# Kernel optimization log

Hardware: AMD Instinct MI355X
Metric: run time of the kernel (lower is better)

The kernel has to match this reference:

```python
import jax, jax.numpy as jnp
import numpy as np

TOP_K = 8


def setup_inputs() -> dict:
    key = jax.random.key(0)
    ks = jax.random.split(key, 7)
    B, D, E = 65536, 1024, 64
    return {
        "x": jax.random.normal(ks[0], (B, D), dtype=jnp.float32),
        "Wg": jax.random.normal(ks[1], (E, D), dtype=jnp.float32) * 0.02,
        "bg": jax.random.normal(ks[2], (E,), dtype=jnp.float32) * 0.02,
        "Wn": jax.random.normal(ks[3], (E, D), dtype=jnp.float32) * 0.02,
        "bn": jax.random.normal(ks[4], (E,), dtype=jnp.float32) * 0.02,
        "We": jax.random.normal(ks[5], (E, D), dtype=jnp.float32) * 0.02,
        "noise": jax.random.normal(ks[6], (B, E), dtype=jnp.float32),
    }


def reference(x, Wg, bg, Wn, bn, We, noise):
    # Router (faithful to original: top-k is taken on noise_logits,
    # and noisy_logits is computed but does not affect the output).
    logits = x @ Wg.T + bg                      # [B, E]
    noise_logits = x @ Wn.T + bn                # [B, E]
    noisy_logits = logits + noise * jax.nn.softplus(noise_logits)  # unused downstream
    del noisy_logits

    top_vals, top_idx = jax.lax.top_k(noise_logits, TOP_K)  # [B, K]
    B, E = noise_logits.shape
    neg_inf = jnp.array(-jnp.inf, dtype=x.dtype)
    sparse_logits = jnp.full((B, E), neg_inf, dtype=x.dtype)
    sparse_logits = sparse_logits.at[jnp.arange(B)[:, None], top_idx].set(top_vals)
    routing_weights = jax.nn.softmax(sparse_logits, axis=-1)  # [B, E]

    # All experts are Linear(d, 1, bias=False): stack into one GEMM.
    expert_out = x @ We.T                        # [B, E]
    final_out = jnp.sum(expert_out * routing_weights, axis=-1, keepdims=True)  # [B, 1]
    return final_out
```

## Files before the change

kernel.cpp:

```cpp
#include <hip/hip_runtime.h>

#define DDIM 1024
#define NEXP 64
#define TOPK 8
#define BK 32
#define ROWS 64
#define NTILE 32
#define TAUF 1.0e-2f
#define TAUB 2.0e-2f

typedef __attribute__((ext_vector_type(8))) short short8;
typedef __attribute__((ext_vector_type(4))) float f32x4;

static __device__ __forceinline__ unsigned int f2u(float f) { return __builtin_bit_cast(unsigned int, f); }
static __device__ __forceinline__ float u2f(unsigned int u) { return __builtin_bit_cast(float, u); }

static __device__ __forceinline__ unsigned short bf_hi_rne(float x) {
    unsigned int u = f2u(x);
    return (unsigned short)((u + (0x7FFFu + ((u >> 16) & 1u))) >> 16);
}

static __device__ __forceinline__ void split2(float x, unsigned short& h, unsigned short& l) {
    unsigned int u = f2u(x);
    unsigned int uh = (u + (0x7FFFu + ((u >> 16) & 1u))) & 0xFFFF0000u;
    h = (unsigned short)(uh >> 16);
    float rem = x - u2f(uh);
    l = (unsigned short)(f2u(rem) >> 16);
}

__global__ __launch_bounds__(256) void conv_w_kernel(
    const float* __restrict__ Wn, const float* __restrict__ We, char* __restrict__ wsW)
{
    int g = blockIdx.x * 256 + threadIdx.x;
    int e = g >> 7, c128 = g & 127;
    int k = c128 << 3;
    int t = k >> 5, c = (k >> 3) & 3;
    const float* np = Wn + (size_t)e * DDIM + k;
    const float* ep = We + (size_t)e * DDIM + k;
    f32x4 n0 = ((const f32x4*)np)[0], n1 = ((const f32x4*)np)[1];
    f32x4 e0 = ((const f32x4*)ep)[0], e1 = ((const f32x4*)ep)[1];
    short8 nh, nl, eh;
#pragma unroll
    for (int i = 0; i < 4; i++) { unsigned short h, l; split2(n0[i], h, l); nh[i] = (short)h; nl[i] = (short)l; }
#pragma unroll
    for (int i = 0; i < 4; i++) { unsigned short h, l; split2(n1[i], h, l); nh[i + 4] = (short)h; nl[i + 4] = (short)l; }
#pragma unroll
    for (int i = 0; i < 4; i++) eh[i] = (short)bf_hi_rne(e0[i]);
#pragma unroll
    for (int i = 0; i < 4; i++) eh[i + 4] = (short)bf_hi_rne(e1[i]);
    size_t dst = (size_t)t * 12288 + (size_t)((e * 64 + c * 16) ^ ((e & 7) << 4));
    *(short8*)(wsW + dst)        = nh;
    *(short8*)(wsW + dst + 4096) = nl;
    *(short8*)(wsW + dst + 8192) = eh;
}

template <int PRE>
__global__ __launch_bounds__(256, 4) void moe_kernel(
    const float* __restrict__ x, const float* __restrict__ Wn,
    const float* __restrict__ bn, const float* __restrict__ We,
    const char* __restrict__ wsW, float* __restrict__ out)
{
    __shared__ __align__(16) char smem[33792];

    const int tid = threadIdx.x;
    const int wid = tid >> 6;
    const int lane = tid & 63;
    const int fr = lane & 15;
    const int fq = lane >> 4;
    const int blockRow = blockIdx.x * ROWS;

    const int srow = tid >> 2, sg = tid & 3;
    const int swz = (srow * 64 + sg * 16) ^ ((srow & 7) << 4);
    const float* xsrc = x + (size_t)(blockRow + srow) * DDIM + sg * 8;

    f32x4 sx0, sx1;
    f32x4 sn0, sn1, se0, se1;

    auto xload = [&](int t) {
        const float* p = xsrc + t * BK;
        sx0 = ((const f32x4*)p)[0];
        sx1 = ((const f32x4*)p)[1];
        if constexpr (!PRE) {
            const float* np = Wn + (size_t)srow * DDIM + t * BK + sg * 8;
            const float* ep = We + (size_t)srow * DDIM + t * BK + sg * 8;
            sn0 = ((const f32x4*)np)[0]; sn1 = ((const f32x4*)np)[1];
            se0 = ((const f32x4*)ep)[0]; se1 = ((const f32x4*)ep)[1];
        }
    };

    auto stage_write = [&](int b) {
        short8 xh;
#pragma unroll
        for (int i = 0; i < 4; i++) xh[i] = (short)bf_hi_rne(sx0[i]);
#pragma unroll
        for (int i = 0; i < 4; i++) xh[i + 4] = (short)bf_hi_rne(sx1[i]);
        *(short8*)(smem + b * 4096 + swz) = xh;
        if constexpr (!PRE) {
            short8 nh, nl, eh;
#pragma unroll
            for (int i = 0; i < 4; i++) { unsigned short h, l; split2(sn0[i], h, l); nh[i] = (short)h; nl[i] = (short)l; }
#pragma unroll
            for (int i = 0; i < 4; i++) { unsigned short h, l; split2(sn1[i], h, l); nh[i + 4] = (short)h; nl[i + 4] = (short)l; }
#pragma unroll
            for (int i = 0; i < 4; i++) eh[i] = (short)bf_hi_rne(se0[i]);
#pragma unroll
            for (int i = 0; i < 4; i++) eh[i + 4] = (short)bf_hi_rne(se1[i]);
            char* wb = smem + 8192 + b * 12288 + swz;
            *(short8*)(wb)        = nh;
            *(short8*)(wb + 4096) = nl;
            *(short8*)(wb + 8192) = eh;
        }
    };

    auto wdma = [&](int t, int b) {
        const char* gs = wsW + (size_t)t * 12288 + wid * 1024 + lane * 16;
        char* ls = smem + 8192 + b * 12288 + wid * 1024;
#pragma unroll
        for (int i = 0; i < 3; i++)
            __builtin_amdgcn_global_load_lds(
                (const __attribute__((address_space(1))) void*)(gs + i * 4096),
                (__attribute__((address_space(3))) void*)(ls + i * 4096), 16, 0, 0);
    };

    f32x4 accN[4], accE[4];
#pragma unroll
    for (int rt = 0; rt < 4; rt++) { accN[rt] = f32x4{0.f,0.f,0.f,0.f}; accE[rt] = f32x4{0.f,0.f,0.f,0.f}; }

    const int ecol = wid * 16 + fr;
    const int woffr = (ecol * 64 + fq * 16) ^ ((ecol & 7) << 4);

    auto compute = [&](int b) {
        const char* wb = smem + 8192 + b * 12288;
        short8 wh = *(const short8*)(wb + woffr);
        short8 wl = *(const short8*)(wb + 4096 + woffr);
        short8 eh = *(const short8*)(wb + 8192 + woffr);
#pragma unroll
        for (int rt = 0; rt < 4; rt++) {
            const int row = rt * 16 + fr;
            const int xoff = (row * 64 + fq * 16) ^ ((row & 7) << 4);
            short8 xh = *(const short8*)(smem + b * 4096 + xoff);
            accN[rt] = __builtin_amdgcn_mfma_f32_16x16x32_bf16(xh, wh, accN[rt], 0, 0, 0);
            accN[rt] = __builtin_amdgcn_mfma_f32_16x16x32_bf16(xh, wl, accN[rt], 0, 0, 0);
            accE[rt] = __builtin_amdgcn_mfma_f32_16x16x32_bf16(xh, eh, accE[rt], 0, 0, 0);
        }
    };

    xload(0);
    if constexpr (PRE) wdma(0, 0);
    stage_write(0);
    xload(1);
    if constexpr (PRE) asm volatile("s_waitcnt vmcnt(2) lgkmcnt(0)" ::: "memory");
    else               asm volatile("s_waitcnt lgkmcnt(0)" ::: "memory");
    __builtin_amdgcn_s_barrier();
    asm volatile("" ::: "memory");

    for (int t = 0; t < NTILE; ++t) {
        const int cur = t & 1, nxt = cur ^ 1;
        if (t + 1 < NTILE) {
            if constexpr (PRE) wdma(t + 1, nxt);
            stage_write(nxt);
            if (t + 2 < NTILE) xload(t + 2);
        }
        compute(cur);
        if (t + 1 < NTILE) {
            if constexpr (PRE) {
                if (t + 2 < NTILE) asm volatile("s_waitcnt vmcnt(2) lgkmcnt(0)" ::: "memory");
                else               asm volatile("s_waitcnt vmcnt(0) lgkmcnt(0)" ::: "memory");
            } else {
                asm volatile("s_waitcnt lgkmcnt(0)" ::: "memory");
            }
            __builtin_amdgcn_s_barrier();
            asm volatile("" ::: "memory");
        }
    }
    __syncthreads();

    float* s_log = (float*)smem;
    float* s_exp = (float*)(smem + 16640);
    float* s_gap = (float*)(smem + 33280);
    float* s_vb  = (float*)(smem + 33536);

    const float be = bn[ecol];
#pragma unroll
    for (int rt = 0; rt < 4; rt++) {
#pragma unroll
        for (int j = 0; j < 4; j++) {
            const int r = rt * 16 + fq * 4 + j;
            s_log[r * 65 + ecol] = accN[rt][j] + be;
            s_exp[r * 65 + ecol] = accE[rt][j];
        }
    }
    __syncthreads();

    auto do_row = [&](int r, float& gapo, float& vbo) -> float {
        float selv[TOPK]; int seli[TOPK];
        unsigned long long chosen = 0ull;
#pragma unroll
        for (int t = 0; t < TOPK; t++) {
            float best = -3.0e38f; int bi = 0;
#pragma unroll 4
            for (int e = 0; e < NEXP; e++) {
                float v = s_log[r * 65 + e];
                if (!((chosen >> e) & 1ull) && v > best) { best = v; bi = e; }
            }
            selv[t] = best; seli[t] = bi; chosen |= (1ull << bi);
        }
        float v9 = -3.0e38f;
#pragma unroll 4
        for (int e = 0; e < NEXP; e++) {
            float v = s_log[r * 65 + e];
            if (!((chosen >> e) & 1ull) && v > v9) v9 = v;
        }
        gapo = selv[TOPK - 1] - v9;
        vbo = 0.5f * (selv[TOPK - 1] + v9);
        float m = selv[0], Z = 0.f, o = 0.f;
#pragma unroll
        for (int t = 0; t < TOPK; t++) {
            float w = __expf(selv[t] - m);
            Z += w;
            o += w * s_exp[r * 65 + seli[t]];
        }
        return o / Z;
    };

    if (lane < 16) {
        const int r = wid * 16 + lane;
        float gap, vb;
        float res = do_row(r, gap, vb);
        out[blockRow + r] = res;
        s_gap[r] = gap; s_vb[r] = vb;
    }
    __syncthreads();

    for (int r = wid; r < ROWS; r += 4) {
        if (!(s_gap[r] < TAUF)) continue;
        const float vbr = s_vb[r];
        const float ve = s_log[r * 65 + lane];
        unsigned long long cand = __ballot(fabsf(ve - vbr) <= TAUB);
        const f32x4* xq = (const f32x4*)(x + (size_t)(blockRow + r) * DDIM) + lane * 4;
        const f32x4 xv0 = xq[0], xv1 = xq[1], xv2 = xq[2], xv3 = xq[3];
        while (cand) {
            const int ce = __builtin_ctzll(cand);
            cand &= cand - 1;
            const f32x4* wq = (const f32x4*)(Wn + (size_t)ce * DDIM) + lane * 4;
            const f32x4 w0 = wq[0], w1 = wq[1], w2 = wq[2], w3 = wq[3];
            double s = 0.0;
#pragma unroll
            for (int i = 0; i < 4; i++) s = fma((double)xv0[i], (double)w0[i], s);
#pragma unroll
            for (int i = 0; i < 4; i++) s = fma((double)xv1[i], (double)w1[i], s);
#pragma unroll
            for (int i = 0; i < 4; i++) s = fma((double)xv2[i], (double)w2[i], s);
#pragma unroll
            for (int i = 0; i < 4; i++) s = fma((double)xv3[i], (double)w3[i], s);
#pragma unroll
            for (int off = 32; off > 0; off >>= 1) s += __shfl_xor(s, off);
            s += (double)bn[ce];
            if (lane == 0) s_log[r * 65 + ce] = (float)s;
        }
    }
    __syncthreads();

    if (lane < 16) {
        const int r = wid * 16 + lane;
        if (s_gap[r] < TAUF) {
            float g2, v2;
            out[blockRow + r] = do_row(r, g2, v2);
        }
    }
}

extern "C" void kernel_launch(void* const* d_in, const int* in_sizes, int n_in,
                              void* d_out, int out_size, void* d_ws, size_t ws_size,
                              hipStream_t stream)
{
    const float* x  = (const float*)d_in[0];
    const float* Wn = (const float*)d_in[3];
    const float* bn = (const float*)d_in[4];
    const float* We = (const float*)d_in[5];
    float* out = (float*)d_out;

    const int B = in_sizes[0] / DDIM;
    const int grid = B / ROWS;

    const size_t need = (size_t)NTILE * 12288;
    if (d_ws != nullptr && ws_size >= need) {
        conv_w_kernel<<<(NEXP * DDIM / 8) / 256, 256, 0, stream>>>(Wn, We, (char*)d_ws);
        moe_kernel<1><<<grid, 256, 0, stream>>>(x, Wn, bn, We, (const char*)d_ws, out);
    } else {
        moe_kernel<0><<<grid, 256, 0, stream>>>(x, Wn, bn, We, nullptr, out);
    }
}
```

Before: 135.4 us.

## Load expert weight fragments directly into registers instead of staging through LDS

The weight tiles (hi/lo noise weights and expert weights) are now laid out in the prepacked workspace so each lane can load its MFMA B-fragment straight from global memory into registers. This removes the global-to-LDS DMA path and the LDS reads. The main loop is rewritten as a manually double-buffered register pipeline using macros, and only x is still staged through LDS. The fallback thresholds TAUF/TAUB are also halved, which changes how often the exact-recheck path is taken. The risks are extra VGPR pressure and redundant global/L2 traffic, since every block reloads the weights directly.

```diff
diff --git a/kernel.cpp b/kernel.cpp
--- a/kernel.cpp
+++ b/kernel.cpp
@@ -6,8 +6,8 @@
 #define BK 32
 #define ROWS 64
 #define NTILE 32
-#define TAUF 1.0e-2f
-#define TAUB 2.0e-2f
+#define TAUF 5.0e-3f
+#define TAUB 1.0e-2f
 
 typedef __attribute__((ext_vector_type(8))) short short8;
 typedef __attribute__((ext_vector_type(4))) float f32x4;
@@ -48,10 +48,10 @@
     for (int i = 0; i < 4; i++) eh[i] = (short)bf_hi_rne(e0[i]);
 #pragma unroll
     for (int i = 0; i < 4; i++) eh[i + 4] = (short)bf_hi_rne(e1[i]);
-    size_t dst = (size_t)t * 12288 + (size_t)((e * 64 + c * 16) ^ ((e & 7) << 4));
+    size_t dst = (size_t)t * 12288 + (size_t)(e >> 4) * 3072 + (size_t)((c * 16 + (e & 15)) * 16);
     *(short8*)(wsW + dst)        = nh;
-    *(short8*)(wsW + dst + 4096) = nl;
-    *(short8*)(wsW + dst + 8192) = eh;
+    *(short8*)(wsW + dst + 1024) = nl;
+    *(short8*)(wsW + dst + 2048) = eh;
 }
 
 template <int PRE>
@@ -73,104 +73,76 @@
     const int swz = (srow * 64 + sg * 16) ^ ((srow & 7) << 4);
     const float* xsrc = x + (size_t)(blockRow + srow) * DDIM + sg * 8;
 
-    f32x4 sx0, sx1;
-    f32x4 sn0, sn1, se0, se1;
-
-    auto xload = [&](int t) {
-        const float* p = xsrc + t * BK;
-        sx0 = ((const f32x4*)p)[0];
-        sx1 = ((const f32x4*)p)[1];
-        if constexpr (!PRE) {
-            const float* np = Wn + (size_t)srow * DDIM + t * BK + sg * 8;
-            const float* ep = We + (size_t)srow * DDIM + t * BK + sg * 8;
-            sn0 = ((const f32x4*)np)[0]; sn1 = ((const f32x4*)np)[1];
-            se0 = ((const f32x4*)ep)[0]; se1 = ((const f32x4*)ep)[1];
-        }
-    };
-
-    auto stage_write = [&](int b) {
-        short8 xh;
-#pragma unroll
-        for (int i = 0; i < 4; i++) xh[i] = (short)bf_hi_rne(sx0[i]);
-#pragma unroll
-        for (int i = 0; i < 4; i++) xh[i + 4] = (short)bf_hi_rne(sx1[i]);
-        *(short8*)(smem + b * 4096 + swz) = xh;
-        if constexpr (!PRE) {
-            short8 nh, nl, eh;
-#pragma unroll
-            for (int i = 0; i < 4; i++) { unsigned short h, l; split2(sn0[i], h, l); nh[i] = (short)h; nl[i] = (short)l; }
-#pragma unroll
-            for (int i = 0; i < 4; i++) { unsigned short h, l; split2(sn1[i], h, l); nh[i + 4] = (short)h; nl[i + 4] = (short)l; }
-#pragma unroll
-            for (int i = 0; i < 4; i++) eh[i] = (short)bf_hi_rne(se0[i]);
-#pragma unroll
-            for (int i = 0; i < 4; i++) eh[i + 4] = (short)bf_hi_rne(se1[i]);
-            char* wb = smem + 8192 + b * 12288 + swz;
-            *(short8*)(wb)        = nh;
-            *(short8*)(wb + 4096) = nl;
-            *(short8*)(wb + 8192) = eh;
-        }
-    };
-
-    auto wdma = [&](int t, int b) {
-        const char* gs = wsW + (size_t)t * 12288 + wid * 1024 + lane * 16;
-        char* ls = smem + 8192 + b * 12288 + wid * 1024;
-#pragma unroll
-        for (int i = 0; i < 3; i++)
-            __builtin_amdgcn_global_load_lds(
-                (const __attribute__((address_space(1))) void*)(gs + i * 4096),
-                (__attribute__((address_space(3))) void*)(ls + i * 4096), 16, 0, 0);
-    };
+    f32x4 sxA0, sxA1, sxB0, sxB1;
+    short8 whA, wlA, ehA, whB, wlB, ehB;
+
+    const char* wbase = wsW + wid * 3072 + lane * 16;
+
+#define XLOAD_A(t) { const float* p = xsrc + (t) * BK; sxA0 = ((const f32x4*)p)[0]; sxA1 = ((const f32x4*)p)[1]; }
+#define XLOAD_B(t) { const float* p = xsrc + (t) * BK; sxB0 = ((const f32x4*)p)[0]; sxB1 = ((const f32x4*)p)[1]; }
+
+#define WLOAD(t, wh, wl, eh) { \
+    if constexpr (PRE) { \
+        const char* wp = wbase + (size_t)(t) * 12288; \
+        wh = *(const short8*)(wp); \
+        wl = *(const short8*)(wp + 1024); \
+        eh = *(const short8*)(wp + 2048); \
+    } else { \
+        const float* np = Wn + (size_t)(wid * 16 + fr) * DDIM + (t) * BK + fq * 8; \
+        const float* ep = We + (size_t)(wid * 16 + fr) * DDIM + (t) * BK + fq * 8; \
+        f32x4 n0 = ((const f32x4*)np)[0], n1 = ((const f32x4*)np)[1]; \
+        f32x4 e0 = ((const f32x4*)ep)[0], e1 = ((const f32x4*)ep)[1]; \
+        for (int i = 0; i < 4; i++) { unsigned short h, l; split2(n0[i], h, l); wh[i] = (short)h; wl[i] = (short)l; } \
+        for (int i = 0; i < 4; i++) { unsigned short h, l; split2(n1[i], h, l); wh[i + 4] = (short)h; wl[i + 4] = (short)l; } \
+        for (int i = 0; i < 4; i++) eh[i] = (short)bf_hi_rne(e0[i]); \
+        for (int i = 0; i < 4; i++) eh[i + 4] = (short)bf_hi_rne(e1[i]); \
+    } }
+
+#define STAGE_WRITE(b, s0, s1) { \
+    short8 xh; \
+    for (int i = 0; i < 4; i++) xh[i] = (short)bf_hi_rne(s0[i]); \
+    for (int i = 0; i < 4; i++) xh[i + 4] = (short)bf_hi_rne(s1[i]); \
+    *(short8*)(smem + (b) * 4096 + swz) = xh; }
 
     f32x4 accN[4], accE[4];
 #pragma unroll
     for (int rt = 0; rt < 4; rt++) { accN[rt] = f32x4{0.f,0.f,0.f,0.f}; accE[rt] = f32x4{0.f,0.f,0.f,0.f}; }
 
-    const int ecol = wid * 16 + fr;
-    const int woffr = (ecol * 64 + fq * 16) ^ ((ecol & 7) << 4);
-
-    auto compute = [&](int b) {
-        const char* wb = smem + 8192 + b * 12288;
-        short8 wh = *(const short8*)(wb + woffr);
-        short8 wl = *(const short8*)(wb + 4096 + woffr);
-        short8 eh = *(const short8*)(wb + 8192 + woffr);
-#pragma unroll
-        for (int rt = 0; rt < 4; rt++) {
-            const int row = rt * 16 + fr;
-            const int xoff = (row * 64 + fq * 16) ^ ((row & 7) << 4);
-            short8 xh = *(const short8*)(smem + b * 4096 + xoff);
-            accN[rt] = __builtin_amdgcn_mfma_f32_16x16x32_bf16(xh, wh, accN[rt], 0, 0, 0);
-            accN[rt] = __builtin_amdgcn_mfma_f32_16x16x32_bf16(xh, wl, accN[rt], 0, 0, 0);
-            accE[rt] = __builtin_amdgcn_mfma_f32_16x16x32_bf16(xh, eh, accE[rt], 0, 0, 0);
-        }
-    };
-
-    xload(0);
-    if constexpr (PRE) wdma(0, 0);
-    stage_write(0);
-    xload(1);
-    if constexpr (PRE) asm volatile("s_waitcnt vmcnt(2) lgkmcnt(0)" ::: "memory");
-    else               asm volatile("s_waitcnt lgkmcnt(0)" ::: "memory");
-    __builtin_amdgcn_s_barrier();
-    asm volatile("" ::: "memory");
-
-    for (int t = 0; t < NTILE; ++t) {
-        const int cur = t & 1, nxt = cur ^ 1;
-        if (t + 1 < NTILE) {
-            if constexpr (PRE) wdma(t + 1, nxt);
-            stage_write(nxt);
-            if (t + 2 < NTILE) xload(t + 2);
-        }
-        compute(cur);
-        if (t + 1 < NTILE) {
-            if constexpr (PRE) {
-                if (t + 2 < NTILE) asm volatile("s_waitcnt vmcnt(2) lgkmcnt(0)" ::: "memory");
-                else               asm volatile("s_waitcnt vmcnt(0) lgkmcnt(0)" ::: "memory");
-            } else {
-                asm volatile("s_waitcnt lgkmcnt(0)" ::: "memory");
-            }
-            __builtin_amdgcn_s_barrier();
-            asm volatile("" ::: "memory");
+#define COMPUTE(b, wh, wl, eh) { \
+    const char* xb = smem + (b) * 4096; \
+    _Pragma("unroll") \
+    for (int rt = 0; rt < 4; rt++) { \
+        const int row = rt * 16 + fr; \
+        const int xoff = (row * 64 + fq * 16) ^ ((row & 7) << 4); \
+        short8 xh = *(const short8*)(xb + xoff); \
+        accN[rt] = __builtin_amdgcn_mfma_f32_16x16x32_bf16(xh, wh, accN[rt], 0, 0, 0); \
+        accN[rt] = __builtin_amdgcn_mfma_f32_16x16x32_bf16(xh, wl, accN[rt], 0, 0, 0); \
+        accE[rt] = __builtin_amdgcn_mfma_f32_16x16x32_bf16(xh, eh, accE[rt], 0, 0, 0); \
+    } }
+
+#define BAR() { asm volatile("s_waitcnt lgkmcnt(0)" ::: "memory"); \
+                __builtin_amdgcn_s_barrier(); \
+                asm volatile("" ::: "memory"); }
+
+    XLOAD_A(0); WLOAD(0, whA, wlA, ehA);
+    XLOAD_B(1); WLOAD(1, whB, wlB, ehB);
+    STAGE_WRITE(0, sxA0, sxA1);
+    XLOAD_A(2);
+    BAR();
+
+    for (int p = 0; p < NTILE / 2; ++p) {
+        const int t0 = 2 * p, t1 = 2 * p + 1;
+        COMPUTE(0, whA, wlA, ehA);
+        STAGE_WRITE(1, sxB0, sxB1);
+        if (t0 + 3 < NTILE) XLOAD_B(t0 + 3);
+        if (t0 + 2 < NTILE) WLOAD(t0 + 2, whA, wlA, ehA);
+        BAR();
+        COMPUTE(1, whB, wlB, ehB);
+        if (t1 + 1 < NTILE) {
+            STAGE_WRITE(0, sxA0, sxA1);
+            if (t1 + 3 < NTILE) XLOAD_A(t1 + 3);
+            WLOAD(t1 + 2, whB, wlB, ehB);
+            BAR();
         }
     }
     __syncthreads();
@@ -180,6 +152,7 @@
     float* s_gap = (float*)(smem + 33280);
     float* s_vb  = (float*)(smem + 33536);
 
+    const int ecol = wid * 16 + fr;
     const float be = bn[ecol];
 #pragma unroll
     for (int rt = 0; rt < 4; rt++) {
```

Measured after the change: 126.9 us. 6.3% less time.
